# Optimization experiments

Measured on AMD Instinct MI355X. Metric: run time of the kernel, lower is better.

## Reference

```python
import jax, jax.numpy as jnp
import numpy as np

VOCAB, EMB, UNITS = 32000, 300, 512
B, T = 64, 512


def _gru_scan(x_seq, h0, U, xW_bias):
    # x_seq already projected: xW_bias = x@W + b_in, shape [T, B, 3*UNITS]
    b_rec = xW_bias["b_rec"]
    xw = xW_bias["xw"]

    def step(h, xw_t):
        rec = h @ U + b_rec                       # [B, 3U]
        xz, xr, xh = jnp.split(xw_t, 3, axis=-1)
        rz, rr, rh = jnp.split(rec, 3, axis=-1)
        z = jax.nn.sigmoid(xz + rz)
        r = jax.nn.sigmoid(xr + rr)
        hh = jnp.tanh(xh + r * rh)                # reset_after=True
        h_new = z * h + (1.0 - z) * hh
        return h_new, h_new

    hT, ys = jax.lax.scan(step, h0, xw)
    return ys, hT


def _gru_dir(x_tbe, W, U, b):
    # b: [2, 3U] -> input bias, recurrent bias (Keras reset_after=True)
    xw = x_tbe @ W + b[0]                          # [T, B, 3U] precomputed
    h0 = jnp.zeros((x_tbe.shape[1], U.shape[0]), x_tbe.dtype)
    return _gru_scan(x_tbe, h0, U, {"xw": xw, "b_rec": b[1]})


def setup_inputs() -> dict:
    key = jax.random.key(0)
    ks = jax.random.split(key, 7)
    s_in = 1.0 / np.sqrt(EMB)
    s_rec = 1.0 / np.sqrt(UNITS)
    return {
        "tokens": jax.random.randint(ks[0], (B, T), 0, VOCAB, dtype=jnp.int32),
        "emb_table": jax.random.normal(ks[1], (VOCAB, EMB), jnp.float32) * 0.1,
        "W_f": jax.random.normal(ks[2], (EMB, 3 * UNITS), jnp.float32) * s_in,
        "U_f": jax.random.normal(ks[3], (UNITS, 3 * UNITS), jnp.float32) * s_rec,
        "b_f": jnp.zeros((2, 3 * UNITS), jnp.float32),
        "W_b": jax.random.normal(ks[4], (EMB, 3 * UNITS), jnp.float32) * s_in,
        "U_b": jax.random.normal(ks[5], (UNITS, 3 * UNITS), jnp.float32) * s_rec,
        "b_b": jnp.zeros((2, 3 * UNITS), jnp.float32),
    }


def reference(tokens, emb_table, W_f, U_f, b_f, W_b, U_b, b_b):
    x = emb_table[tokens]                          # [B, T, E]
    x_tbe = jnp.transpose(x, (1, 0, 2))            # [T, B, E]
    ys_f, h_f = _gru_dir(x_tbe, W_f, U_f, b_f)
    ys_b, h_b = _gru_dir(x_tbe[::-1], W_b, U_b, b_b)
    ys_b = ys_b[::-1]
    output = jnp.transpose(jnp.concatenate([ys_f, ys_b], -1), (1, 0, 2))  # [B,T,2U]
    state = jnp.concatenate([h_f, h_b], -1)        # [B, 2U]
    return output, state
```

## Files before the change

kernel.cpp:

```cpp
#include <hip/hip_runtime.h>
#include <math.h>

#define TT   512
#define BB   64
#define EMBD 300
#define NU   512
#define G3   1536

static constexpr size_t XW_FLOATS = (size_t)2 * TT * BB * G3;
static constexpr size_t HB_FLOATS = (size_t)2 * 2 * BB * NU;

__global__ __launch_bounds__(256) void k_input_gemm(
    const int* __restrict__ tokens, const float* __restrict__ emb,
    const float* __restrict__ Wf, const float* __restrict__ bf,
    const float* __restrict__ Wb, const float* __restrict__ bb,
    float* __restrict__ xw) {
  __shared__ float As[8][72];
  __shared__ float Bs[8][64];
  __shared__ int tok[64];
  const int t = blockIdx.y;
  const int n0 = blockIdx.x * 64;
  const int dir = blockIdx.z;
  const float* W = dir ? Wb : Wf;
  const float* bias = dir ? bb : bf;
  float* out = xw + (size_t)dir * TT * BB * G3;
  const int tid = threadIdx.x;
  if (tid < 64) tok[tid] = tokens[(size_t)tid * TT + t];
  __syncthreads();
  const int tx = tid & 15, ty = tid >> 4;
  float4 c0 = {0,0,0,0}, c1 = {0,0,0,0}, c2 = {0,0,0,0}, c3 = {0,0,0,0};
  for (int kc = 0; kc < 38; ++kc) {
    const int k0 = kc * 8;
    if (tid < 128) {
      int kb = tid >> 4, nq = (tid & 15) * 4;
      float4 v = {0,0,0,0};
      if (k0 + kb < EMBD) v = *(const float4*)(W + (size_t)(k0 + kb) * G3 + n0 + nq);
      *(float4*)&Bs[kb][nq] = v;
    } else {
      int th = tid - 128;
      int b = th >> 1, kh = (th & 1) * 4;
      float4 v = {0,0,0,0};
      if (k0 + kh + 4 <= EMBD) v = *(const float4*)(emb + (size_t)tok[b] * EMBD + k0 + kh);
      As[kh + 0][b] = v.x; As[kh + 1][b] = v.y; As[kh + 2][b] = v.z; As[kh + 3][b] = v.w;
    }
    __syncthreads();
    #pragma unroll
    for (int kb = 0; kb < 8; ++kb) {
      float4 bv = *(const float4*)&Bs[kb][tx * 4];
      float4 av = *(const float4*)&As[kb][ty * 4];
      c0.x = fmaf(av.x, bv.x, c0.x); c0.y = fmaf(av.x, bv.y, c0.y);
      c0.z = fmaf(av.x, bv.z, c0.z); c0.w = fmaf(av.x, bv.w, c0.w);
      c1.x = fmaf(av.y, bv.x, c1.x); c1.y = fmaf(av.y, bv.y, c1.y);
      c1.z = fmaf(av.y, bv.z, c1.z); c1.w = fmaf(av.y, bv.w, c1.w);
      c2.x = fmaf(av.z, bv.x, c2.x); c2.y = fmaf(av.z, bv.y, c2.y);
      c2.z = fmaf(av.z, bv.z, c2.z); c2.w = fmaf(av.z, bv.w, c2.w);
      c3.x = fmaf(av.w, bv.x, c3.x); c3.y = fmaf(av.w, bv.y, c3.y);
      c3.z = fmaf(av.w, bv.z, c3.z); c3.w = fmaf(av.w, bv.w, c3.w);
    }
    __syncthreads();
  }
  float4 bi = *(const float4*)(bias + n0 + tx * 4);
  size_t base = ((size_t)t * BB + (size_t)ty * 4) * G3 + n0 + tx * 4;
  float4 o;
  o.x = c0.x + bi.x; o.y = c0.y + bi.y; o.z = c0.z + bi.z; o.w = c0.w + bi.w;
  *(float4*)(out + base) = o;
  o.x = c1.x + bi.x; o.y = c1.y + bi.y; o.z = c1.z + bi.z; o.w = c1.w + bi.w;
  *(float4*)(out + base + G3) = o;
  o.x = c2.x + bi.x; o.y = c2.y + bi.y; o.z = c2.z + bi.z; o.w = c2.w + bi.w;
  *(float4*)(out + base + 2 * G3) = o;
  o.x = c3.x + bi.x; o.y = c3.y + bi.y; o.z = c3.z + bi.z; o.w = c3.w + bi.w;
  *(float4*)(out + base + 3 * G3) = o;
}

__global__ __launch_bounds__(256, 1) void k_gru(
    const float* __restrict__ xw,
    const float* __restrict__ Uf, const float* __restrict__ Ub,
    const float* __restrict__ bf, const float* __restrict__ bb,
    float* __restrict__ hbuf, int* __restrict__ ctr,
    float* __restrict__ out, float* __restrict__ state) {
  __shared__ float hS[8][NU];
  __shared__ float red[3][8][8][32];
  const int wg = blockIdx.x;
  const int dir = wg >> 7;
  const int bblk = (wg >> 4) & 7;
  const int ublk = wg & 15;
  const int u0 = ublk * 32, b0 = bblk * 8;
  int* gctr = ctr + (dir * 8 + bblk) * 32;
  const int tid = threadIdx.x;
  const int u = tid & 31;
  const int hi = tid >> 5;
  const int kb0 = hi * 64;
  const float* xwd = xw + (size_t)dir * TT * BB * G3;
  const float* U = dir ? Ub : Uf;
  const float* br = (dir ? bb : bf) + G3;
  const float brz = br[u0 + u], brr = br[512 + u0 + u], brh = br[1024 + u0 + u];
  float* hb = hbuf + (size_t)dir * 2 * BB * NU;

  float Uz_r[64], Ur_r[64], Uh_r[64];
  #pragma unroll
  for (int kk = 0; kk < 64; ++kk) {
    const float* row = U + (size_t)(kb0 + kk) * G3 + u0 + u;
    Uz_r[kk] = row[0];
    Ur_r[kk] = row[512];
    Uh_r[kk] = row[1024];
  }
  #pragma unroll
  for (int kk = 0; kk < 64; ++kk) {
    asm volatile("" : "+v"(Uz_r[kk]), "+v"(Ur_r[kk]), "+v"(Uh_r[kk]));
  }

  #pragma unroll
  for (int j = 0; j < 16; ++j) hS[hi][u + j * 32] = 0.f;
  __syncthreads();

  for (int s = 0; s < TT; ++s) {
    const int t = dir ? (TT - 1 - s) : s;
    const float* xp = xwd + ((size_t)t * BB + b0 + hi) * G3 + u0 + u;
    const float xz = xp[0], xr = xp[512], xh = xp[1024];
    float az[8], ar[8], ah[8];
    #pragma unroll
    for (int b = 0; b < 8; ++b) { az[b] = 0.f; ar[b] = 0.f; ah[b] = 0.f; }
    #pragma unroll
    for (int q = 0; q < 16; ++q) {
      #pragma unroll
      for (int b = 0; b < 8; ++b) {
        float4 hv = *(const float4*)&hS[b][kb0 + q * 4];
        az[b] = fmaf(Uz_r[q*4+0], hv.x, az[b]); az[b] = fmaf(Uz_r[q*4+1], hv.y, az[b]);
        az[b] = fmaf(Uz_r[q*4+2], hv.z, az[b]); az[b] = fmaf(Uz_r[q*4+3], hv.w, az[b]);
        ar[b] = fmaf(Ur_r[q*4+0], hv.x, ar[b]); ar[b] = fmaf(Ur_r[q*4+1], hv.y, ar[b]);
        ar[b] = fmaf(Ur_r[q*4+2], hv.z, ar[b]); ar[b] = fmaf(Ur_r[q*4+3], hv.w, ar[b]);
        ah[b] = fmaf(Uh_r[q*4+0], hv.x, ah[b]); ah[b] = fmaf(Uh_r[q*4+1], hv.y, ah[b]);
        ah[b] = fmaf(Uh_r[q*4+2], hv.z, ah[b]); ah[b] = fmaf(Uh_r[q*4+3], hv.w, ah[b]);
      }
    }
    #pragma unroll
    for (int b = 0; b < 8; ++b) {
      red[0][b][hi][u] = az[b];
      red[1][b][hi][u] = ar[b];
      red[2][b][hi][u] = ah[b];
    }
    __syncthreads();
    float rz = 0.f, rr = 0.f, rh = 0.f;
    #pragma unroll
    for (int q = 0; q < 8; ++q) {
      rz += red[0][hi][q][u];
      rr += red[1][hi][q][u];
      rh += red[2][hi][q][u];
    }
    const int bg = b0 + hi;
    const float z = 1.f / (1.f + __expf(-(xz + rz + brz)));
    const float r = 1.f / (1.f + __expf(-(xr + rr + brr)));
    const float hh = tanhf(xh + r * (rh + brh));
    const float hold = hS[hi][u0 + u];
    const float hn = z * hold + (1.f - z) * hh;
    __hip_atomic_store(hb + ((size_t)(s & 1) * BB + bg) * NU + u0 + u, hn,
                       __ATOMIC_RELAXED, __HIP_MEMORY_SCOPE_AGENT);
    out[((size_t)bg * TT + t) * 1024 + (size_t)dir * NU + u0 + u] = hn;
    if (s == TT - 1) {
      state[(size_t)bg * 1024 + (size_t)dir * NU + u0 + u] = hn;
    } else {
      __syncthreads();
      if (tid == 0) {
        __hip_atomic_fetch_add(gctr, 1, __ATOMIC_RELEASE, __HIP_MEMORY_SCOPE_AGENT);
        const int target = 16 * (s + 1);
        while (__hip_atomic_load(gctr, __ATOMIC_RELAXED, __HIP_MEMORY_SCOPE_AGENT) < target) {
          __builtin_amdgcn_s_sleep(2);
        }
      }
      __syncthreads();
      const float* hsrc = hb + (size_t)(s & 1) * BB * NU;
      #pragma unroll
      for (int j = 0; j < 4; ++j) {
        int fi = tid + j * 256;
        int bl = fi >> 7, k4 = (fi & 127) * 4;
        const float* p = hsrc + (size_t)(b0 + bl) * NU + k4;
        float v0 = __hip_atomic_load((float*)(p + 0), __ATOMIC_RELAXED, __HIP_MEMORY_SCOPE_AGENT);
        float v1 = __hip_atomic_load((float*)(p + 1), __ATOMIC_RELAXED, __HIP_MEMORY_SCOPE_AGENT);
        float v2 = __hip_atomic_load((float*)(p + 2), __ATOMIC_RELAXED, __HIP_MEMORY_SCOPE_AGENT);
        float v3 = __hip_atomic_load((float*)(p + 3), __ATOMIC_RELAXED, __HIP_MEMORY_SCOPE_AGENT);
        float* d = &hS[bl][k4];
        d[0] = v0; d[1] = v1; d[2] = v2; d[3] = v3;
      }
      __syncthreads();
    }
  }
}

extern "C" void kernel_launch(void* const* d_in, const int* in_sizes, int n_in,
                              void* d_out, int out_size, void* d_ws, size_t ws_size,
                              hipStream_t stream) {
  (void)in_sizes; (void)n_in; (void)out_size; (void)ws_size;
  const int*   tokens = (const int*)d_in[0];
  const float* emb    = (const float*)d_in[1];
  const float* Wf     = (const float*)d_in[2];
  const float* Uf     = (const float*)d_in[3];
  const float* bf     = (const float*)d_in[4];
  const float* Wb     = (const float*)d_in[5];
  const float* Ub     = (const float*)d_in[6];
  const float* bb     = (const float*)d_in[7];
  float* ws = (float*)d_ws;
  float* xw = ws;
  float* hb = ws + XW_FLOATS;
  int*   ctr = (int*)(hb + HB_FLOATS);
  float* out = (float*)d_out;
  float* state = out + (size_t)BB * TT * 1024;

  hipMemsetAsync(ctr, 0, 16 * 32 * sizeof(int), stream);
  hipLaunchKernelGGL(k_input_gemm, dim3(24, 512, 2), dim3(256), 0, stream,
                     tokens, emb, Wf, bf, Wb, bb, xw);
  hipLaunchKernelGGL(k_gru, dim3(256), dim3(256), 0, stream,
                     xw, Uf, Ub, bf, bb, hb, ctr, out, state);
}
```

Measured before the change: 6.198 ms.

## Split GRU recurrence across twice as many workgroups with swizzled LDS and prefetch

The persistent GRU kernel now launches 512 workgroups instead of 256. Each handles 16 units rather than 32 with a 32-wide K slice per thread group, which halves the U-register footprint and allows two workgroups per CU. The hidden-state LDS layout is XOR-swizzled to cut bank conflicts, and h is fetched with 64-bit atomic loads. The next step's input projection is prefetched before the barrier, and the previous h is kept in a register instead of read from LDS. The trade-off is that each group barrier now waits on 32 arrivals instead of 16, and the gate math runs on only half the threads.

```diff
diff --git a/kernel.cpp b/kernel.cpp
--- a/kernel.cpp
+++ b/kernel.cpp
@@ -1,5 +1,6 @@
 #include <hip/hip_runtime.h>
 #include <math.h>
+#include <stdint.h>
 
 #define TT   512
 #define BB   64
@@ -72,59 +73,72 @@
   *(float4*)(out + base + 3 * G3) = o;
 }
 
-__global__ __launch_bounds__(256, 1) void k_gru(
+__global__ __launch_bounds__(256, 2) void k_gru(
     const float* __restrict__ xw,
     const float* __restrict__ Uf, const float* __restrict__ Ub,
     const float* __restrict__ bf, const float* __restrict__ bb,
     float* __restrict__ hbuf, int* __restrict__ ctr,
     float* __restrict__ out, float* __restrict__ state) {
   __shared__ float hS[8][NU];
-  __shared__ float red[3][8][8][32];
+  __shared__ float red[3][8][17][16];
   const int wg = blockIdx.x;
-  const int dir = wg >> 7;
-  const int bblk = (wg >> 4) & 7;
-  const int ublk = wg & 15;
-  const int u0 = ublk * 32, b0 = bblk * 8;
-  int* gctr = ctr + (dir * 8 + bblk) * 32;
+  const int lo4 = wg & 15, mid4 = (wg >> 4) & 15, hi1 = wg >> 8;
+  const int gid  = lo4 ^ mid4 ^ (hi1 ? 15 : 0);
+  const int ublk = (hi1 << 4) | mid4;
+  const int dir  = gid >> 3;
+  const int bblk = gid & 7;
+  const int u0 = ublk * 16, b0 = bblk * 8;
+  int* gctr = ctr + gid * 32;
   const int tid = threadIdx.x;
-  const int u = tid & 31;
-  const int hi = tid >> 5;
-  const int kb0 = hi * 64;
+  const int u  = tid & 15;
+  const int ks = tid >> 4;
+  const int kb0 = ks * 32;
+  const int swzb = (ks & 7) << 2;
   const float* xwd = xw + (size_t)dir * TT * BB * G3;
   const float* U = dir ? Ub : Uf;
   const float* br = (dir ? bb : bf) + G3;
-  const float brz = br[u0 + u], brr = br[512 + u0 + u], brh = br[1024 + u0 + u];
   float* hb = hbuf + (size_t)dir * 2 * BB * NU;
 
-  float Uz_r[64], Ur_r[64], Uh_r[64];
+  float Uz_r[32], Ur_r[32], Uh_r[32];
   #pragma unroll
-  for (int kk = 0; kk < 64; ++kk) {
+  for (int kk = 0; kk < 32; ++kk) {
     const float* row = U + (size_t)(kb0 + kk) * G3 + u0 + u;
     Uz_r[kk] = row[0];
     Ur_r[kk] = row[512];
     Uh_r[kk] = row[1024];
   }
   #pragma unroll
-  for (int kk = 0; kk < 64; ++kk) {
+  for (int kk = 0; kk < 32; ++kk) {
     asm volatile("" : "+v"(Uz_r[kk]), "+v"(Ur_r[kk]), "+v"(Uh_r[kk]));
   }
 
+  const int eb = tid >> 4;
+  const int eu = tid & 15;
+  float brz = 0.f, brr = 0.f, brh = 0.f, hprev = 0.f;
+  float xz = 0.f, xr = 0.f, xh = 0.f;
+  if (tid < 128) {
+    brz = br[u0 + eu]; brr = br[512 + u0 + eu]; brh = br[1024 + u0 + eu];
+    const int t0 = dir ? (TT - 1) : 0;
+    const float* xp = xwd + ((size_t)t0 * BB + b0 + eb) * G3 + u0 + eu;
+    xz = xp[0]; xr = xp[512]; xh = xp[1024];
+  }
+
+  float* hflat = &hS[0][0];
   #pragma unroll
-  for (int j = 0; j < 16; ++j) hS[hi][u + j * 32] = 0.f;
+  for (int j = 0; j < 16; ++j) hflat[tid + j * 256] = 0.f;
   __syncthreads();
 
   for (int s = 0; s < TT; ++s) {
     const int t = dir ? (TT - 1 - s) : s;
-    const float* xp = xwd + ((size_t)t * BB + b0 + hi) * G3 + u0 + u;
-    const float xz = xp[0], xr = xp[512], xh = xp[1024];
     float az[8], ar[8], ah[8];
     #pragma unroll
     for (int b = 0; b < 8; ++b) { az[b] = 0.f; ar[b] = 0.f; ah[b] = 0.f; }
     #pragma unroll
-    for (int q = 0; q < 16; ++q) {
+    for (int q = 0; q < 8; ++q) {
+      const int col = kb0 + ((q << 2) ^ swzb);
       #pragma unroll
       for (int b = 0; b < 8; ++b) {
-        float4 hv = *(const float4*)&hS[b][kb0 + q * 4];
+        float4 hv = *(const float4*)&hS[b][col];
         az[b] = fmaf(Uz_r[q*4+0], hv.x, az[b]); az[b] = fmaf(Uz_r[q*4+1], hv.y, az[b]);
         az[b] = fmaf(Uz_r[q*4+2], hv.z, az[b]); az[b] = fmaf(Uz_r[q*4+3], hv.w, az[b]);
         ar[b] = fmaf(Ur_r[q*4+0], hv.x, ar[b]); ar[b] = fmaf(Ur_r[q*4+1], hv.y, ar[b]);
@@ -135,51 +149,59 @@
     }
     #pragma unroll
     for (int b = 0; b < 8; ++b) {
-      red[0][b][hi][u] = az[b];
-      red[1][b][hi][u] = ar[b];
-      red[2][b][hi][u] = ah[b];
+      red[0][b][ks][u] = az[b];
+      red[1][b][ks][u] = ar[b];
+      red[2][b][ks][u] = ah[b];
     }
     __syncthreads();
-    float rz = 0.f, rr = 0.f, rh = 0.f;
-    #pragma unroll
-    for (int q = 0; q < 8; ++q) {
-      rz += red[0][hi][q][u];
-      rr += red[1][hi][q][u];
-      rh += red[2][hi][q][u];
-    }
-    const int bg = b0 + hi;
-    const float z = 1.f / (1.f + __expf(-(xz + rz + brz)));
-    const float r = 1.f / (1.f + __expf(-(xr + rr + brr)));
-    const float hh = tanhf(xh + r * (rh + brh));
-    const float hold = hS[hi][u0 + u];
-    const float hn = z * hold + (1.f - z) * hh;
-    __hip_atomic_store(hb + ((size_t)(s & 1) * BB + bg) * NU + u0 + u, hn,
-                       __ATOMIC_RELAXED, __HIP_MEMORY_SCOPE_AGENT);
-    out[((size_t)bg * TT + t) * 1024 + (size_t)dir * NU + u0 + u] = hn;
+    float hn = 0.f;
+    if (tid < 128) {
+      float rz = 0.f, rr = 0.f, rh = 0.f;
+      #pragma unroll
+      for (int q2 = 0; q2 < 16; ++q2) {
+        rz += red[0][eb][q2][eu];
+        rr += red[1][eb][q2][eu];
+        rh += red[2][eb][q2][eu];
+      }
+      const float z  = 1.f / (1.f + __expf(-(xz + rz + brz)));
+      const float r  = 1.f / (1.f + __expf(-(xr + rr + brr)));
+      const float hh = tanhf(xh + r * (rh + brh));
+      hn = z * hprev + (1.f - z) * hh;
+      hprev = hn;
+      __hip_atomic_store(hb + ((size_t)(s & 1) * BB + b0 + eb) * NU + u0 + eu, hn,
+                         __ATOMIC_RELAXED, __HIP_MEMORY_SCOPE_AGENT);
+      __builtin_nontemporal_store(
+          hn, out + ((size_t)(b0 + eb) * TT + t) * 1024 + (size_t)dir * NU + u0 + eu);
+    }
     if (s == TT - 1) {
-      state[(size_t)bg * 1024 + (size_t)dir * NU + u0 + u] = hn;
+      if (tid < 128)
+        state[(size_t)(b0 + eb) * 1024 + (size_t)dir * NU + u0 + eu] = hn;
     } else {
+      if (tid < 128) {
+        const int tn = dir ? (TT - 2 - s) : (s + 1);
+        const float* xp = xwd + ((size_t)tn * BB + b0 + eb) * G3 + u0 + eu;
+        xz = xp[0]; xr = xp[512]; xh = xp[1024];
+      }
       __syncthreads();
       if (tid == 0) {
         __hip_atomic_fetch_add(gctr, 1, __ATOMIC_RELEASE, __HIP_MEMORY_SCOPE_AGENT);
-        const int target = 16 * (s + 1);
+        const int target = 32 * (s + 1);
         while (__hip_atomic_load(gctr, __ATOMIC_RELAXED, __HIP_MEMORY_SCOPE_AGENT) < target) {
           __builtin_amdgcn_s_sleep(2);
         }
       }
       __syncthreads();
-      const float* hsrc = hb + (size_t)(s & 1) * BB * NU;
+      const uint64_t* hsrc = (const uint64_t*)(hb + (size_t)(s & 1) * BB * NU);
       #pragma unroll
-      for (int j = 0; j < 4; ++j) {
-        int fi = tid + j * 256;
-        int bl = fi >> 7, k4 = (fi & 127) * 4;
-        const float* p = hsrc + (size_t)(b0 + bl) * NU + k4;
-        float v0 = __hip_atomic_load((float*)(p + 0), __ATOMIC_RELAXED, __HIP_MEMORY_SCOPE_AGENT);
-        float v1 = __hip_atomic_load((float*)(p + 1), __ATOMIC_RELAXED, __HIP_MEMORY_SCOPE_AGENT);
-        float v2 = __hip_atomic_load((float*)(p + 2), __ATOMIC_RELAXED, __HIP_MEMORY_SCOPE_AGENT);
-        float v3 = __hip_atomic_load((float*)(p + 3), __ATOMIC_RELAXED, __HIP_MEMORY_SCOPE_AGENT);
-        float* d = &hS[bl][k4];
-        d[0] = v0; d[1] = v1; d[2] = v2; d[3] = v3;
+      for (int j = 0; j < 8; ++j) {
+        const int fi = tid + j * 256;
+        const int bl = fi >> 8;
+        const int k2 = fi & 255;
+        const int k  = k2 * 2;
+        uint64_t v = __hip_atomic_load(hsrc + ((size_t)(b0 + bl) << 8) + k2,
+                                       __ATOMIC_RELAXED, __HIP_MEMORY_SCOPE_AGENT);
+        const int c = k ^ (((k >> 5) & 7) << 2);
+        *(uint64_t*)&hS[bl][c] = v;
       }
       __syncthreads();
     }
@@ -208,6 +230,6 @@
   hipMemsetAsync(ctr, 0, 16 * 32 * sizeof(int), stream);
   hipLaunchKernelGGL(k_input_gemm, dim3(24, 512, 2), dim3(256), 0, stream,
                      tokens, emb, Wf, bf, Wb, bb, xw);
-  hipLaunchKernelGGL(k_gru, dim3(256), dim3(256), 0, stream,
+  hipLaunchKernelGGL(k_gru, dim3(512), dim3(256), 0, stream,
                      xw, Uf, Ub, bf, bb, hb, ctr, out, state);
 }
```

Result: slower. 10.67 ms (+72.1%).

## Replace counter barrier with per-block flags and prefetch next-step inputs

Applied to the files above, without the earlier changes.

Each workgroup now publishes a per-block step flag instead of atomically incrementing a shared counter. The wait is done by one wavefront polling all 16 flags with a wave vote. The next timestep's input projection is prefetched and the output store is issued before the wait, as a nontemporal store. The h exchange switches to 64-bit atomic loads and the h store to atomic exchange, trading memory-ordering subtlety (relaxed flags with no release) for lower barrier latency on the serial recurrence.

```diff
diff --git a/kernel.cpp b/kernel.cpp
--- a/kernel.cpp
+++ b/kernel.cpp
@@ -1,5 +1,6 @@
 #include <hip/hip_runtime.h>
 #include <math.h>
+#include <stdint.h>
 
 #define TT   512
 #define BB   64
@@ -85,7 +86,8 @@
   const int bblk = (wg >> 4) & 7;
   const int ublk = wg & 15;
   const int u0 = ublk * 32, b0 = bblk * 8;
-  int* gctr = ctr + (dir * 8 + bblk) * 32;
+  const int gid = dir * 8 + bblk;
+  int* flags = ctr + gid * 16;
   const int tid = threadIdx.x;
   const int u = tid & 31;
   const int hi = tid >> 5;
@@ -113,10 +115,15 @@
   for (int j = 0; j < 16; ++j) hS[hi][u + j * 32] = 0.f;
   __syncthreads();
 
+  float xz, xr, xh;
+  {
+    const int t0 = dir ? (TT - 1) : 0;
+    const float* xp = xwd + ((size_t)t0 * BB + b0 + hi) * G3 + u0 + u;
+    xz = xp[0]; xr = xp[512]; xh = xp[1024];
+  }
+
   for (int s = 0; s < TT; ++s) {
     const int t = dir ? (TT - 1 - s) : s;
-    const float* xp = xwd + ((size_t)t * BB + b0 + hi) * G3 + u0 + u;
-    const float xz = xp[0], xr = xp[512], xh = xp[1024];
     float az[8], ar[8], ah[8];
     #pragma unroll
     for (int b = 0; b < 8; ++b) { az[b] = 0.f; ar[b] = 0.f; ah[b] = 0.f; }
@@ -153,33 +160,49 @@
     const float hh = tanhf(xh + r * (rh + brh));
     const float hold = hS[hi][u0 + u];
     const float hn = z * hold + (1.f - z) * hh;
-    __hip_atomic_store(hb + ((size_t)(s & 1) * BB + bg) * NU + u0 + u, hn,
-                       __ATOMIC_RELAXED, __HIP_MEMORY_SCOPE_AGENT);
-    out[((size_t)bg * TT + t) * 1024 + (size_t)dir * NU + u0 + u] = hn;
+    {
+      float oldv = __hip_atomic_exchange(
+          hb + ((size_t)(s & 1) * BB + bg) * NU + u0 + u, hn,
+          __ATOMIC_RELAXED, __HIP_MEMORY_SCOPE_AGENT);
+      asm volatile("" :: "v"(oldv));
+    }
     if (s == TT - 1) {
+      out[((size_t)bg * TT + t) * 1024 + (size_t)dir * NU + u0 + u] = hn;
       state[(size_t)bg * 1024 + (size_t)dir * NU + u0 + u] = hn;
     } else {
       __syncthreads();
       if (tid == 0) {
-        __hip_atomic_fetch_add(gctr, 1, __ATOMIC_RELEASE, __HIP_MEMORY_SCOPE_AGENT);
-        const int target = 16 * (s + 1);
-        while (__hip_atomic_load(gctr, __ATOMIC_RELAXED, __HIP_MEMORY_SCOPE_AGENT) < target) {
-          __builtin_amdgcn_s_sleep(2);
+        __hip_atomic_exchange(flags + ublk, s + 1,
+                              __ATOMIC_RELAXED, __HIP_MEMORY_SCOPE_AGENT);
+      }
+      __builtin_nontemporal_store(
+          hn, out + ((size_t)bg * TT + t) * 1024 + (size_t)dir * NU + u0 + u);
+      {
+        const int tn = dir ? (TT - 2 - s) : (s + 1);
+        const float* xp = xwd + ((size_t)tn * BB + b0 + hi) * G3 + u0 + u;
+        xz = xp[0]; xr = xp[512]; xh = xp[1024];
+      }
+      if (tid < 64) {
+        const int target = s + 1;
+        int f = target;
+        for (;;) {
+          if (tid < 16)
+            f = __hip_atomic_load(flags + tid, __ATOMIC_RELAXED,
+                                  __HIP_MEMORY_SCOPE_AGENT);
+          if (__all(f >= target)) break;
+          __builtin_amdgcn_s_sleep(1);
         }
       }
       __syncthreads();
-      const float* hsrc = hb + (size_t)(s & 1) * BB * NU;
+      const uint64_t* hsrc = (const uint64_t*)(hb + (size_t)(s & 1) * BB * NU);
       #pragma unroll
-      for (int j = 0; j < 4; ++j) {
-        int fi = tid + j * 256;
-        int bl = fi >> 7, k4 = (fi & 127) * 4;
-        const float* p = hsrc + (size_t)(b0 + bl) * NU + k4;
-        float v0 = __hip_atomic_load((float*)(p + 0), __ATOMIC_RELAXED, __HIP_MEMORY_SCOPE_AGENT);
-        float v1 = __hip_atomic_load((float*)(p + 1), __ATOMIC_RELAXED, __HIP_MEMORY_SCOPE_AGENT);
-        float v2 = __hip_atomic_load((float*)(p + 2), __ATOMIC_RELAXED, __HIP_MEMORY_SCOPE_AGENT);
-        float v3 = __hip_atomic_load((float*)(p + 3), __ATOMIC_RELAXED, __HIP_MEMORY_SCOPE_AGENT);
-        float* d = &hS[bl][k4];
-        d[0] = v0; d[1] = v1; d[2] = v2; d[3] = v3;
+      for (int j = 0; j < 8; ++j) {
+        const int fi = tid + j * 256;
+        const int bl = fi >> 8;
+        const int k2 = fi & 255;
+        uint64_t v = __hip_atomic_load(hsrc + ((size_t)(b0 + bl) << 8) + k2,
+                                       __ATOMIC_RELAXED, __HIP_MEMORY_SCOPE_AGENT);
+        *(uint64_t*)&hS[bl][k2 * 2] = v;
       }
       __syncthreads();
     }
```

Result: slower. 8.085 ms (+30.4%).
